# Optimization experiments

Measured on AMD Instinct MI355X. Metric: run time of the kernel, lower is better.

Reference implementation:

```python
import jax, jax.numpy as jnp
import numpy as np

N_NODES = 100000
N_EDGES = 1600000
FEAT, HID, OUT = 256, 128, 64
N_BATCH = 10000
EPS = 1e-5


def gcn_conv(x, src, dst, W, b, n):
    # PyG GCNConv: linear -> add self loops -> sym-normalized scatter-add -> bias
    h = x @ W  # [N, C]
    loop = jnp.arange(n, dtype=src.dtype)
    s = jnp.concatenate([src, loop])
    d = jnp.concatenate([dst, loop])
    deg = jax.ops.segment_sum(jnp.ones_like(d, dtype=h.dtype), d, num_segments=n)
    dinv = jnp.where(deg > 0, jax.lax.rsqrt(deg), 0.0)
    norm = dinv[s] * dinv[d]                    # [E+N]
    msg = h[s] * norm[:, None]                  # gather + scale
    out = jax.ops.segment_sum(msg, d, num_segments=n)  # scatter-add
    return out + b


def batch_norm(x, gamma, beta):
    # training-mode BatchNorm1d: batch statistics, biased variance
    mu = jnp.mean(x, axis=0)
    var = jnp.var(x, axis=0)
    return (x - mu) * jax.lax.rsqrt(var + EPS) * gamma + beta


def setup_inputs() -> dict:
    key = jax.random.key(0)
    ks = jax.random.split(key, 8)
    features = jax.random.normal(ks[0], (N_NODES, FEAT), dtype=jnp.float32)
    edge_index = jax.random.randint(ks[1], (2, N_EDGES), 0, N_NODES, dtype=jnp.int64 if jax.config.jax_enable_x64 else jnp.int32)
    batch_nodes = jax.random.randint(ks[2], (N_BATCH,), 0, N_NODES, dtype=jnp.int32)
    W1 = jax.random.normal(ks[3], (FEAT, HID), dtype=jnp.float32) * (1.0 / np.sqrt(FEAT))
    b1 = jnp.zeros((HID,), jnp.float32)
    gamma1 = jnp.ones((HID,), jnp.float32)
    beta1 = jnp.zeros((HID,), jnp.float32)
    W2 = jax.random.normal(ks[4], (HID, OUT), dtype=jnp.float32) * (1.0 / np.sqrt(HID))
    b2 = jnp.zeros((OUT,), jnp.float32)
    gamma2 = jnp.ones((OUT,), jnp.float32)
    beta2 = jnp.zeros((OUT,), jnp.float32)
    return {"features": features, "edge_index": edge_index, "batch_nodes": batch_nodes,
            "W1": W1, "b1": b1, "gamma1": gamma1, "beta1": beta1,
            "W2": W2, "b2": b2, "gamma2": gamma2, "beta2": beta2}


def reference(features, edge_index, batch_nodes, W1, b1, gamma1, beta1, W2, b2, gamma2, beta2):
    src, dst = edge_index[0], edge_index[1]
    n = features.shape[0]
    x = gcn_conv(features, src, dst, W1, b1, n)
    x = jax.nn.relu(batch_norm(x, gamma1, beta1))
    # dropout treated as identity (deterministic reference)
    x = gcn_conv(x, src, dst, W2, b2, n)
    x = jax.nn.relu(batch_norm(x, gamma2, beta2))
    return jax.nn.log_softmax(x[batch_nodes], axis=1)
```

## Files before the change

kernel.cpp:

```cpp
#include <hip/hip_runtime.h>
#include <stdint.h>

typedef unsigned short bf16_t;

constexpr int kNN   = 100000;
constexpr int kNE   = 1600000;
constexpr int kFEAT = 256;
constexpr int kHID  = 128;
constexpr int kOUT  = 64;
constexpr int kNB   = 10000;
constexpr float kEPS = 1e-5f;

constexpr int kEPB  = 4096;
constexpr int kNBLK = (kNE + kEPB - 1) / kEPB;
constexpr int kNBUK = (kNN + 511) / 512;

typedef __attribute__((ext_vector_type(8))) short short8v;
typedef __attribute__((ext_vector_type(4))) float f32x4;

__device__ __forceinline__ float bf2f(bf16_t u) {
    union { uint32_t i; float f; } v; v.i = ((uint32_t)u) << 16; return v.f;
}
__device__ __forceinline__ bf16_t f2bf(float f) {
    uint32_t u = __float_as_uint(f);
    uint32_t r = (u + 0x7FFFu + ((u >> 16) & 1u)) >> 16;
    return (bf16_t)r;
}
__device__ __forceinline__ float lo16(uint32_t u) {
    union { uint32_t i; float f; } v; v.i = u << 16; return v.f;
}
__device__ __forceinline__ float hi16(uint32_t u) {
    union { uint32_t i; float f; } v; v.i = u & 0xFFFF0000u; return v.f;
}

__global__ void k_probe(const uint32_t* __restrict__ feat, const uint32_t* __restrict__ ei,
                        int* __restrict__ flags) {
    int l = threadIdx.x;
    int good = 0;
    for (int j = l; j < 256; j += 64) {
        uint32_t e = (feat[j] >> 7) & 0xFFu;
        if (e >= 100u && e <= 132u) good++;
    }
    for (int o = 32; o; o >>= 1) good += __shfl_xor(good, o);
    int zeros = 0;
    for (int j = l; j < 128; j += 64) zeros += (ei[2 * j + 1] == 0u) ? 1 : 0;
    for (int o = 32; o; o >>= 1) zeros += __shfl_xor(zeros, o);
    if (l == 0) {
        flags[0] = (good > 128) ? 1 : 0;
        flags[1] = (zeros > 64) ? 1 : 0;
    }
}


__global__ void k_hist1(const int* __restrict__ ei, const int* __restrict__ flags,
                        unsigned int* __restrict__ counts) {
    __shared__ unsigned int lh[kNBUK];
    int t = threadIdx.x;
    for (int i = t; i < kNBUK; i += 256) lh[i] = 0u;
    __syncthreads();
    int i64 = flags[1];
    int base = blockIdx.x * kEPB;
    for (int k = 0; k < 16; k++) {
        int e = base + k * 256 + t;
        if (e < kNE) {
            int d = i64 ? ei[2 * (kNE + e)] : ei[kNE + e];
            atomicAdd(&lh[d >> 9], 1u);
        }
    }
    __syncthreads();
    for (int i = t; i < kNBUK; i += 256) counts[(size_t)i * kNBLK + blockIdx.x] = lh[i];
}

__global__ void k_scanA(const unsigned int* __restrict__ counts, unsigned int* __restrict__ base,
                        float* __restrict__ stats) {
    __shared__ unsigned int ss[256];
    int t = threadIdx.x;
    for (int i = t; i < 384; i += 256) stats[i] = 0.f;
    unsigned int tot = 0u;
    if (t < kNBUK) {
        const unsigned int* row = counts + (size_t)t * kNBLK;
        for (int j = 0; j < kNBLK; j++) tot += row[j];
    }
    ss[t] = tot;
    __syncthreads();
    for (int o = 1; o < 256; o <<= 1) {
        unsigned int x = (t >= o) ? ss[t - o] : 0u;
        __syncthreads();
        ss[t] += x;
        __syncthreads();
    }
    if (t < kNBUK) base[t] = ss[t] - tot;
    if (t == 0) base[kNBUK] = ss[255];
}

__global__ void k_scanB(const unsigned int* __restrict__ counts, const unsigned int* __restrict__ base,
                        unsigned int* __restrict__ off) {
    __shared__ unsigned int ss[64];
    int b = blockIdx.x, t = threadIdx.x;
    unsigned int run = base[b];
    for (int c0 = 0; c0 < kNBLK; c0 += 64) {
        int idx = c0 + t;
        unsigned int v = (idx < kNBLK) ? counts[(size_t)b * kNBLK + idx] : 0u;
        ss[t] = v;
        __syncthreads();
        for (int o = 1; o < 64; o <<= 1) {
            unsigned int x = (t >= o) ? ss[t - o] : 0u;
            __syncthreads();
            ss[t] += x;
            __syncthreads();
        }
        if (idx < kNBLK) off[(size_t)b * kNBLK + idx] = run + ss[t] - v;
        unsigned int ctot = ss[63];
        __syncthreads();
        run += ctot;
    }
}

__global__ void k_scatter1(const int* __restrict__ ei, const int* __restrict__ flags,
                           const unsigned int* __restrict__ off, unsigned int* __restrict__ pairs) {
    __shared__ unsigned int lcur[kNBUK];
    int t = threadIdx.x;
    for (int i = t; i < kNBUK; i += 256) lcur[i] = off[(size_t)i * kNBLK + blockIdx.x];
    __syncthreads();
    int i64 = flags[1];
    int base = blockIdx.x * kEPB;
    for (int k = 0; k < 16; k++) {
        int e = base + k * 256 + t;
        if (e < kNE) {
            int s, d;
            if (i64) { s = ei[2 * e]; d = ei[2 * (kNE + e)]; }
            else     { s = ei[e];     d = ei[kNE + e]; }
            unsigned int p = atomicAdd(&lcur[d >> 9], 1u);
            pairs[p] = (unsigned int)s | ((unsigned int)(d & 511) << 17);
        }
    }
}

__global__ void __launch_bounds__(1024) k_scatter2(const unsigned int* __restrict__ pairs,
                        const unsigned int* __restrict__ base, unsigned int* __restrict__ deg,
                        float* __restrict__ dinv, unsigned int* __restrict__ cursor,
                        int* __restrict__ sorted) {
    __shared__ unsigned int hist[512], sc[512], lcur[512];
    int b = blockIdx.x, t = threadIdx.x;
    unsigned int gb = base[b];
    int cnt = (int)(base[b + 1] - gb);
    if (t < 512) hist[t] = 0u;
    __syncthreads();
    for (int i = t; i < cnt; i += 1024) atomicAdd(&hist[pairs[gb + i] >> 17], 1u);
    __syncthreads();
    if (t < 512) sc[t] = hist[t];
    __syncthreads();
    for (int o = 1; o < 512; o <<= 1) {
        unsigned int x = 0u;
        if (t < 512 && t >= o) x = sc[t - o];
        __syncthreads();
        if (t < 512) sc[t] += x;
        __syncthreads();
    }
    if (t < 512) {
        lcur[t] = gb + sc[t] - hist[t];
        int node = b * 512 + t;
        if (node < kNN) {
            unsigned int dg = hist[t] + 1u;
            deg[node] = dg;
            dinv[node] = rsqrtf((float)dg);
            cursor[node] = gb + sc[t];
        }
    }
    __syncthreads();
    for (int i = t; i < cnt; i += 1024) {
        unsigned int pk = pairs[gb + i];
        unsigned int slot = atomicAdd(&lcur[pk >> 17], 1u);
        sorted[slot] = (int)(pk & 0x1FFFFu);
    }
}

__global__ void k_prepw(const void* __restrict__ W1, const void* __restrict__ W2,
                        const int* __restrict__ flags, bf16_t* __restrict__ Wz1,
                        bf16_t* __restrict__ Wz2) {
    int gid = blockIdx.x * 256 + threadIdx.x;
    int isbf = flags[0];
    if (gid < 4096) {
        int idx = gid;
        int l = idx & 63, j = (idx >> 6) & 7, t = idx >> 9;
        int col = j * 16 + (l & 15);
        int kb = t * 32 + (l >> 4) * 8;
        bf16_t o[8];
        if (isbf) {
            const bf16_t* Wb = (const bf16_t*)W1;
            #pragma unroll
            for (int i = 0; i < 8; i++) o[i] = Wb[(size_t)(kb + i) * kHID + col];
        } else {
            const float* Wf = (const float*)W1;
            #pragma unroll
            for (int i = 0; i < 8; i++) o[i] = f2bf(Wf[(size_t)(kb + i) * kHID + col]);
        }
        uint4 w;
        w.x = (uint32_t)o[0] | ((uint32_t)o[1] << 16);
        w.y = (uint32_t)o[2] | ((uint32_t)o[3] << 16);
        w.z = (uint32_t)o[4] | ((uint32_t)o[5] << 16);
        w.w = (uint32_t)o[6] | ((uint32_t)o[7] << 16);
        *(uint4*)(Wz1 + (size_t)idx * 8) = w;
    } else if (gid < 4096 + 1024) {
        int idx = gid - 4096;
        int l = idx & 63, j = (idx >> 6) & 3, t = idx >> 8;
        int col = j * 16 + (l & 15);
        int kb = t * 32 + (l >> 4) * 8;
        bf16_t o[8];
        if (isbf) {
            const bf16_t* Wb = (const bf16_t*)W2;
            #pragma unroll
            for (int i = 0; i < 8; i++) o[i] = Wb[(size_t)(kb + i) * kOUT + col];
        } else {
            const float* Wf = (const float*)W2;
            #pragma unroll
            for (int i = 0; i < 8; i++) o[i] = f2bf(Wf[(size_t)(kb + i) * kOUT + col]);
        }
        uint4 w;
        w.x = (uint32_t)o[0] | ((uint32_t)o[1] << 16);
        w.y = (uint32_t)o[2] | ((uint32_t)o[3] << 16);
        w.z = (uint32_t)o[4] | ((uint32_t)o[5] << 16);
        w.w = (uint32_t)o[6] | ((uint32_t)o[7] << 16);
        *(uint4*)(Wz2 + (size_t)idx * 8) = w;
    }
}

__global__ void k_gemm1(const void* __restrict__ A, const bf16_t* __restrict__ Wz,
                        const float* __restrict__ dinv, bf16_t* __restrict__ H,
                        const int* __restrict__ flags) {
    int isbf = flags[0];
    int wv = threadIdx.x >> 6;
    int l  = threadIdx.x & 63;
    int kgrp = l >> 4;
    int rbase = blockIdx.x * 128 + wv * 32;
    int arow0 = rbase + (l & 15);
    int arow1 = arow0 + 16;
    const bf16_t* Ab = (const bf16_t*)A;
    const float*  Af = (const float*)A;
    const short8v* Wv = (const short8v*)Wz;

    f32x4 acc[2][8];
    #pragma unroll
    for (int m = 0; m < 2; m++)
        #pragma unroll
        for (int j = 0; j < 8; j++)
            acc[m][j] = (f32x4){0.f, 0.f, 0.f, 0.f};

    #pragma unroll
    for (int t = 0; t < 8; t++) {
        int kbase = t * 32 + kgrp * 8;
        short8v a0, a1;
        #pragma unroll
        for (int i = 0; i < 8; i++) { a0[i] = 0; a1[i] = 0; }
        if (arow0 < kNN) {
            if (isbf) {
                a0 = *(const short8v*)(Ab + (size_t)arow0 * kFEAT + kbase);
            } else {
                const float* p = Af + (size_t)arow0 * kFEAT + kbase;
                #pragma unroll
                for (int i = 0; i < 8; i++) a0[i] = (short)f2bf(p[i]);
            }
        }
        if (arow1 < kNN) {
            if (isbf) {
                a1 = *(const short8v*)(Ab + (size_t)arow1 * kFEAT + kbase);
            } else {
                const float* p = Af + (size_t)arow1 * kFEAT + kbase;
                #pragma unroll
                for (int i = 0; i < 8; i++) a1[i] = (short)f2bf(p[i]);
            }
        }
        #pragma unroll
        for (int j = 0; j < 8; j++) {
            short8v b = Wv[(t * 8 + j) * 64 + l];
            acc[0][j] = __builtin_amdgcn_mfma_f32_16x16x32_bf16(a0, b, acc[0][j], 0, 0, 0);
            acc[1][j] = __builtin_amdgcn_mfma_f32_16x16x32_bf16(a1, b, acc[1][j], 0, 0, 0);
        }
    }

    #pragma unroll
    for (int m = 0; m < 2; m++) {
        #pragma unroll
        for (int r = 0; r < 4; r++) {
            int orow = rbase + m * 16 + kgrp * 4 + r;
            if (orow < kNN) {
                float dn = dinv[orow];
                bf16_t* hp = H + (size_t)orow * kHID + (l & 15);
                #pragma unroll
                for (int j = 0; j < 8; j++) hp[j * 16] = f2bf(acc[m][j][r] * dn);
            }
        }
    }
}

__global__ void k_agg1(const bf16_t* __restrict__ H, const int* __restrict__ sorted,
                       const unsigned int* __restrict__ cursor, const unsigned int* __restrict__ deg,
                       const float* __restrict__ dinv, const void* __restrict__ bias,
                       const int* __restrict__ flags, float* __restrict__ Out) {
    int t = threadIdx.x;
    int wv = t >> 6;
    int lane = t & 63;
    int c0 = lane * 2;
    int n = blockIdx.x * 4 + wv;
    float b0, b1v;
    if (flags[0]) { b0 = bf2f(((const bf16_t*)bias)[c0]); b1v = bf2f(((const bf16_t*)bias)[c0 + 1]); }
    else          { b0 = ((const float*)bias)[c0];        b1v = ((const float*)bias)[c0 + 1]; }
    const uint32_t* Hrow = (const uint32_t*)H;
    float dn = dinv[n];
    uint32_t hu = Hrow[(size_t)n * 64 + lane];
    float acc0 = lo16(hu), acc1 = hi16(hu);
    unsigned int e1 = cursor[n];
    int cnt = (int)(deg[n] - 1u);
    unsigned int e = e1 - (unsigned int)cnt;
    for (; cnt >= 8; cnt -= 8, e += 8) {
        int s0 = sorted[e],     s1 = sorted[e + 1], s2 = sorted[e + 2], s3 = sorted[e + 3];
        int s4 = sorted[e + 4], s5 = sorted[e + 5], s6 = sorted[e + 6], s7 = sorted[e + 7];
        uint32_t u0 = Hrow[(size_t)s0 * 64 + lane];
        uint32_t u1 = Hrow[(size_t)s1 * 64 + lane];
        uint32_t u2 = Hrow[(size_t)s2 * 64 + lane];
        uint32_t u3 = Hrow[(size_t)s3 * 64 + lane];
        uint32_t u4 = Hrow[(size_t)s4 * 64 + lane];
        uint32_t u5 = Hrow[(size_t)s5 * 64 + lane];
        uint32_t u6 = Hrow[(size_t)s6 * 64 + lane];
        uint32_t u7 = Hrow[(size_t)s7 * 64 + lane];
        acc0 += lo16(u0) + lo16(u1) + lo16(u2) + lo16(u3)
              + lo16(u4) + lo16(u5) + lo16(u6) + lo16(u7);
        acc1 += hi16(u0) + hi16(u1) + hi16(u2) + hi16(u3)
              + hi16(u4) + hi16(u5) + hi16(u6) + hi16(u7);
    }
    for (; cnt > 0; cnt--, e++) {
        uint32_t u = Hrow[(size_t)sorted[e] * 64 + lane];
        acc0 += lo16(u);
        acc1 += hi16(u);
    }
    float2 o; o.x = acc0 * dn + b0; o.y = acc1 * dn + b1v;
    *(float2*)(Out + (size_t)n * kHID + c0) = o;
}

__global__ void k_stat1(const float* __restrict__ A1, float* __restrict__ stats) {
    int c = threadIdx.x & 127;
    int r0 = threadIdx.x >> 7;
    int chunk = (kNN + gridDim.x - 1) / gridDim.x;
    int nbeg = blockIdx.x * chunk;
    int nend = nbeg + chunk; if (nend > kNN) nend = kNN;
    float s0 = 0.f, s1 = 0.f;
    for (int n = nbeg + r0; n < nend; n += 2) {
        float v = A1[(size_t)n * kHID + c];
        s0 += v; s1 += v * v;
    }
    atomicAdd(&stats[c], s0);
    atomicAdd(&stats[kHID + c], s1);
}

__global__ void k_bnprep(const float* __restrict__ stats, const void* __restrict__ gamma,
                         const void* __restrict__ beta, const int* __restrict__ flags,
                         float* __restrict__ bnp) {
    int c = threadIdx.x;
    float mu = stats[c] * (1.f / kNN);
    float var = stats[128 + c] * (1.f / kNN) - mu * mu;
    float rs = rsqrtf(var + kEPS);
    float g, b;
    if (flags[0]) { g = bf2f(((const bf16_t*)gamma)[c]); b = bf2f(((const bf16_t*)beta)[c]); }
    else          { g = ((const float*)gamma)[c];        b = ((const float*)beta)[c]; }
    float sc = rs * g;
    bnp[c] = sc;
    bnp[128 + c] = b - mu * sc;
}

__global__ void k_gemm2(const float* A, const bf16_t* __restrict__ Wz,
                        const float* __restrict__ dinv, const float* __restrict__ bnp,
                        bf16_t* H ) {
    int wv = threadIdx.x >> 6;
    int l  = threadIdx.x & 63;
    int kgrp = l >> 4;
    int rbase = blockIdx.x * 128 + wv * 32;
    int arow0 = rbase + (l & 15);
    int arow1 = arow0 + 16;
    const short8v* Wv = (const short8v*)Wz;

    f32x4 acc[2][4];
    #pragma unroll
    for (int m = 0; m < 2; m++)
        #pragma unroll
        for (int j = 0; j < 4; j++)
            acc[m][j] = (f32x4){0.f, 0.f, 0.f, 0.f};

    #pragma unroll
    for (int t = 0; t < 4; t++) {
        int kbase = t * 32 + kgrp * 8;
        float4 sa = *(const float4*)(bnp + kbase);
        float4 sb = *(const float4*)(bnp + kbase + 4);
        float4 ha = *(const float4*)(bnp + 128 + kbase);
        float4 hb = *(const float4*)(bnp + 128 + kbase + 4);
        short8v a0, a1;
        #pragma unroll
        for (int i = 0; i < 8; i++) { a0[i] = 0; a1[i] = 0; }
        if (arow0 < kNN) {
            float4 f0 = *(const float4*)(A + (size_t)arow0 * kHID + kbase);
            float4 f1 = *(const float4*)(A + (size_t)arow0 * kHID + kbase + 4);
            float v;
            v = f0.x * sa.x + ha.x; a0[0] = (short)f2bf(v > 0.f ? v : 0.f);
            v = f0.y * sa.y + ha.y; a0[1] = (short)f2bf(v > 0.f ? v : 0.f);
            v = f0.z * sa.z + ha.z; a0[2] = (short)f2bf(v > 0.f ? v : 0.f);
            v = f0.w * sa.w + ha.w; a0[3] = (short)f2bf(v > 0.f ? v : 0.f);
            v = f1.x * sb.x + hb.x; a0[4] = (short)f2bf(v > 0.f ? v : 0.f);
            v = f1.y * sb.y + hb.y; a0[5] = (short)f2bf(v > 0.f ? v : 0.f);
            v = f1.z * sb.z + hb.z; a0[6] = (short)f2bf(v > 0.f ? v : 0.f);
            v = f1.w * sb.w + hb.w; a0[7] = (short)f2bf(v > 0.f ? v : 0.f);
        }
        if (arow1 < kNN) {
            float4 f0 = *(const float4*)(A + (size_t)arow1 * kHID + kbase);
            float4 f1 = *(const float4*)(A + (size_t)arow1 * kHID + kbase + 4);
            float v;
            v = f0.x * sa.x + ha.x; a1[0] = (short)f2bf(v > 0.f ? v : 0.f);
            v = f0.y * sa.y + ha.y; a1[1] = (short)f2bf(v > 0.f ? v : 0.f);
            v = f0.z * sa.z + ha.z; a1[2] = (short)f2bf(v > 0.f ? v : 0.f);
            v = f0.w * sa.w + ha.w; a1[3] = (short)f2bf(v > 0.f ? v : 0.f);
            v = f1.x * sb.x + hb.x; a1[4] = (short)f2bf(v > 0.f ? v : 0.f);
            v = f1.y * sb.y + hb.y; a1[5] = (short)f2bf(v > 0.f ? v : 0.f);
            v = f1.z * sb.z + hb.z; a1[6] = (short)f2bf(v > 0.f ? v : 0.f);
            v = f1.w * sb.w + hb.w; a1[7] = (short)f2bf(v > 0.f ? v : 0.f);
        }
        #pragma unroll
        for (int j = 0; j < 4; j++) {
            short8v b = Wv[(t * 4 + j) * 64 + l];
            acc[0][j] = __builtin_amdgcn_mfma_f32_16x16x32_bf16(a0, b, acc[0][j], 0, 0, 0);
            acc[1][j] = __builtin_amdgcn_mfma_f32_16x16x32_bf16(a1, b, acc[1][j], 0, 0, 0);
        }
    }

    #pragma unroll
    for (int m = 0; m < 2; m++) {
        #pragma unroll
        for (int r = 0; r < 4; r++) {
            int orow = rbase + m * 16 + kgrp * 4 + r;
            if (orow < kNN) {
                float dn = dinv[orow];
                bf16_t* hp = H + (size_t)orow * 256 + (l & 15);
                #pragma unroll
                for (int j = 0; j < 4; j++) hp[j * 16] = f2bf(acc[m][j][r] * dn);
            }
        }
    }
}

__global__ void k_agg2(const bf16_t* __restrict__ H, const int* __restrict__ sorted,
                       const unsigned int* __restrict__ cursor, const unsigned int* __restrict__ deg,
                       const float* __restrict__ dinv, const void* __restrict__ bias,
                       const int* __restrict__ flags, float* __restrict__ Out) {
    int t = threadIdx.x;
    int grp = t >> 5;
    int lane = t & 31;
    int c0 = lane * 2;
    int n = blockIdx.x * 8 + grp;
    float b0, b1v;
    if (flags[0]) { b0 = bf2f(((const bf16_t*)bias)[c0]); b1v = bf2f(((const bf16_t*)bias)[c0 + 1]); }
    else          { b0 = ((const float*)bias)[c0];        b1v = ((const float*)bias)[c0 + 1]; }
    const uint32_t* Hrow = (const uint32_t*)H;
    float dn = dinv[n];
    uint32_t hu = Hrow[(size_t)n * 128 + lane];
    float acc0 = lo16(hu), acc1 = hi16(hu);
    unsigned int e1 = cursor[n];
    int cnt = (int)(deg[n] - 1u);
    unsigned int e = e1 - (unsigned int)cnt;
    for (; cnt >= 8; cnt -= 8, e += 8) {
        int s0 = sorted[e],     s1 = sorted[e + 1], s2 = sorted[e + 2], s3 = sorted[e + 3];
        int s4 = sorted[e + 4], s5 = sorted[e + 5], s6 = sorted[e + 6], s7 = sorted[e + 7];
        uint32_t u0 = Hrow[(size_t)s0 * 128 + lane];
        uint32_t u1 = Hrow[(size_t)s1 * 128 + lane];
        uint32_t u2 = Hrow[(size_t)s2 * 128 + lane];
        uint32_t u3 = Hrow[(size_t)s3 * 128 + lane];
        uint32_t u4 = Hrow[(size_t)s4 * 128 + lane];
        uint32_t u5 = Hrow[(size_t)s5 * 128 + lane];
        uint32_t u6 = Hrow[(size_t)s6 * 128 + lane];
        uint32_t u7 = Hrow[(size_t)s7 * 128 + lane];
        acc0 += lo16(u0) + lo16(u1) + lo16(u2) + lo16(u3)
              + lo16(u4) + lo16(u5) + lo16(u6) + lo16(u7);
        acc1 += hi16(u0) + hi16(u1) + hi16(u2) + hi16(u3)
              + hi16(u4) + hi16(u5) + hi16(u6) + hi16(u7);
    }
    for (; cnt > 0; cnt--, e++) {
        uint32_t u = Hrow[(size_t)sorted[e] * 128 + lane];
        acc0 += lo16(u);
        acc1 += hi16(u);
    }
    float2 o; o.x = acc0 * dn + b0; o.y = acc1 * dn + b1v;
    *(float2*)(Out + (size_t)n * kOUT + c0) = o;
}

__global__ void k_stat2(const float* __restrict__ A2, float* __restrict__ stats) {
    int c = threadIdx.x & 63;
    int r0 = threadIdx.x >> 6;
    int chunk = (kNN + gridDim.x - 1) / gridDim.x;
    int nbeg = blockIdx.x * chunk;
    int nend = nbeg + chunk; if (nend > kNN) nend = kNN;
    float s0 = 0.f, s1 = 0.f;
    for (int n = nbeg + r0; n < nend; n += 4) {
        float v = A2[(size_t)n * kOUT + c];
        s0 += v; s1 += v * v;
    }
    atomicAdd(&stats[256 + c], s0);
    atomicAdd(&stats[320 + c], s1);
}

__global__ void k_out(const float* __restrict__ A2, const float* __restrict__ stats,
                      const int* __restrict__ batch, const void* __restrict__ gamma,
                      const void* __restrict__ beta, const int* __restrict__ flags,
                      bf16_t* __restrict__ out) {
    int wid = threadIdx.x >> 6;
    int lane = threadIdx.x & 63;
    int i = blockIdx.x * 4 + wid;
    if (i >= kNB) return;
    int n = batch[i];
    int c = lane;
    float mu = stats[256 + c] * (1.f / kNN);
    float var = stats[320 + c] * (1.f / kNN) - mu * mu;
    float g, b;
    if (flags[0]) { g = bf2f(((const bf16_t*)gamma)[c]); b = bf2f(((const bf16_t*)beta)[c]); }
    else          { g = ((const float*)gamma)[c];        b = ((const float*)beta)[c]; }
    float v = (A2[(size_t)n * kOUT + c] - mu) * rsqrtf(var + kEPS) * g + b;
    v = v > 0.f ? v : 0.f;
    float m = v;
    for (int o = 32; o; o >>= 1) m = fmaxf(m, __shfl_xor(m, o));
    float ex = expf(v - m);
    float s = ex;
    for (int o = 32; o; o >>= 1) s += __shfl_xor(s, o);
    float r = v - m - logf(s);
    if (flags[0]) out[(size_t)i * kOUT + c] = f2bf(r);
    else ((float*)out)[(size_t)i * kOUT + c] = r;
}

static inline size_t align_up(size_t x, size_t a) { return (x + a - 1) & ~(a - 1); }

extern "C" void kernel_launch(void* const* d_in, const int* in_sizes, int n_in,
                              void* d_out, int out_size, void* d_ws, size_t ws_size,
                              hipStream_t stream) {
    (void)in_sizes; (void)n_in; (void)out_size; (void)ws_size;
    const void* feat = d_in[0];
    const int* ei    = (const int*)d_in[1];
    const int* batch = (const int*)d_in[2];
    const void* W1   = d_in[3];
    const void* b1   = d_in[4];
    const void* g1   = d_in[5];
    const void* be1  = d_in[6];
    const void* W2   = d_in[7];
    const void* b2   = d_in[8];
    const void* g2   = d_in[9];
    const void* be2  = d_in[10];

    char* ws = (char*)d_ws;
    size_t o = 0;
    int*          flags  = (int*)(ws + o);          o = align_up(o + 32, 256);
    unsigned int* deg    = (unsigned int*)(ws + o); o = align_up(o + (size_t)kNN * 4, 256);
    float*        dinv   = (float*)(ws + o);        o = align_up(o + (size_t)kNN * 4, 256);
    unsigned int* cursor = (unsigned int*)(ws + o); o = align_up(o + (size_t)kNN * 4, 256);
    float*        stats  = (float*)(ws + o);        o = align_up(o + 384 * 4, 256);
    float*        bnp    = (float*)(ws + o);        o = align_up(o + 256 * 4, 256);
    int*          sorted = (int*)(ws + o);          o = align_up(o + (size_t)kNE * 4, 256);
    bf16_t*       h1     = (bf16_t*)(ws + o);       o = align_up(o + (size_t)kNN * kHID * 2, 256);
    float*        a1     = (float*)(ws + o);        o = align_up(o + (size_t)kNN * kHID * 4, 256);
    bf16_t*       wz1    = (bf16_t*)(ws + o);       o = align_up(o + (size_t)8 * 8 * 64 * 8 * 2, 256);
    bf16_t*       wz2    = (bf16_t*)(ws + o);       o = align_up(o + (size_t)4 * 4 * 64 * 8 * 2, 256);

    unsigned int* pairs  = (unsigned int*)h1;
    unsigned int* counts = (unsigned int*)a1;
    unsigned int* offm   = (unsigned int*)((char*)a1 + 512 * 1024);
    unsigned int* gbase  = (unsigned int*)((char*)a1 + 1024 * 1024);

    bf16_t*       h2 = (bf16_t*)a1;
    float*        a2 = (float*)h1;

    bf16_t* outp = (bf16_t*)d_out;

    k_probe   <<<1, 64, 0, stream>>>((const uint32_t*)feat, (const uint32_t*)ei, flags);
    k_prepw   <<<20, 256, 0, stream>>>(W1, W2, flags, wz1, wz2);
    k_hist1   <<<kNBLK, 256, 0, stream>>>(ei, flags, counts);
    k_scanA   <<<1, 256, 0, stream>>>(counts, gbase, stats);
    k_scanB   <<<kNBUK, 64, 0, stream>>>(counts, gbase, offm);
    k_scatter1<<<kNBLK, 256, 0, stream>>>(ei, flags, offm, pairs);
    k_scatter2<<<kNBUK, 1024, 0, stream>>>(pairs, gbase, deg, dinv, cursor, sorted);

    k_gemm1 <<<(kNN + 127) / 128, 256, 0, stream>>>(feat, wz1, dinv, h1, flags);
    k_agg1  <<<kNN / 4, 256, 0, stream>>>(h1, sorted, cursor, deg, dinv, b1, flags, a1);
    k_stat1 <<<256, 256, 0, stream>>>(a1, stats);
    k_bnprep<<<1, 128, 0, stream>>>(stats, g1, be1, flags, bnp);

    k_gemm2<<<(kNN + 127) / 128, 256, 0, stream>>>(a1, wz2, dinv, bnp, h2);
    k_agg2 <<<kNN / 8, 256, 0, stream>>>(h2, sorted, cursor, deg, dinv, b2, flags, a2);
    k_stat2<<<256, 256, 0, stream>>>(a2, stats);

    k_out<<<(kNB + 3) / 4, 256, 0, stream>>>(a2, stats, batch, g2, be2, flags, outp);
}
```

Baseline: 501.8 us.

## Fuse dtype probe into weight prep and split agg2 edges across half-waves

Removes the separate single-block probe launch by having every k_prepw block recompute the dtype check, with block 0 writing the flags. k_agg2 now assigns one node per full 64-lane wave instead of per 32-lane half, and each half gathers alternate neighbours. The partial sums are combined with a cross-half shuffle. The node index is made wave-uniform with readfirstlane in both aggregation kernels. The goal is more outstanding memory requests per node and one fewer launch, at the cost of twice as many waves for agg2 and some redundant probe reads.

```diff
diff --git a/kernel.cpp b/kernel.cpp
--- a/kernel.cpp
+++ b/kernel.cpp
@@ -31,24 +31,6 @@
 }
 __device__ __forceinline__ float hi16(uint32_t u) {
     union { uint32_t i; float f; } v; v.i = u & 0xFFFF0000u; return v.f;
-}
-
-__global__ void k_probe(const uint32_t* __restrict__ feat, const uint32_t* __restrict__ ei,
-                        int* __restrict__ flags) {
-    int l = threadIdx.x;
-    int good = 0;
-    for (int j = l; j < 256; j += 64) {
-        uint32_t e = (feat[j] >> 7) & 0xFFu;
-        if (e >= 100u && e <= 132u) good++;
-    }
-    for (int o = 32; o; o >>= 1) good += __shfl_xor(good, o);
-    int zeros = 0;
-    for (int j = l; j < 128; j += 64) zeros += (ei[2 * j + 1] == 0u) ? 1 : 0;
-    for (int o = 32; o; o >>= 1) zeros += __shfl_xor(zeros, o);
-    if (l == 0) {
-        flags[0] = (good > 128) ? 1 : 0;
-        flags[1] = (zeros > 64) ? 1 : 0;
-    }
 }
 
 
@@ -176,15 +158,32 @@
 }
 
 __global__ void k_prepw(const void* __restrict__ W1, const void* __restrict__ W2,
-                        const int* __restrict__ flags, bf16_t* __restrict__ Wz1,
+                        const uint32_t* __restrict__ feat, const uint32_t* __restrict__ ei,
+                        int* __restrict__ flags, bf16_t* __restrict__ Wz1,
                         bf16_t* __restrict__ Wz2) {
-    int gid = blockIdx.x * 256 + threadIdx.x;
-    int isbf = flags[0];
+    int t = threadIdx.x;
+    int good = 0;
+    for (int j = t & 63; j < 256; j += 64) {
+        uint32_t ex = (feat[j] >> 7) & 0xFFu;
+        if (ex >= 100u && ex <= 132u) good++;
+    }
+    for (int o = 32; o; o >>= 1) good += __shfl_xor(good, o);
+    int isbf = (good > 128) ? 1 : 0;
+    if (blockIdx.x == 0) {
+        int zeros = 0;
+        for (int j = t & 63; j < 128; j += 64) zeros += (ei[2 * j + 1] == 0u) ? 1 : 0;
+        for (int o = 32; o; o >>= 1) zeros += __shfl_xor(zeros, o);
+        if (t == 0) {
+            flags[0] = isbf;
+            flags[1] = (zeros > 64) ? 1 : 0;
+        }
+    }
+    int gid = blockIdx.x * 256 + t;
     if (gid < 4096) {
         int idx = gid;
-        int l = idx & 63, j = (idx >> 6) & 7, t = idx >> 9;
+        int l = idx & 63, j = (idx >> 6) & 7, tt = idx >> 9;
         int col = j * 16 + (l & 15);
-        int kb = t * 32 + (l >> 4) * 8;
+        int kb = tt * 32 + (l >> 4) * 8;
         bf16_t o[8];
         if (isbf) {
             const bf16_t* Wb = (const bf16_t*)W1;
@@ -203,9 +202,9 @@
         *(uint4*)(Wz1 + (size_t)idx * 8) = w;
     } else if (gid < 4096 + 1024) {
         int idx = gid - 4096;
-        int l = idx & 63, j = (idx >> 6) & 3, t = idx >> 8;
+        int l = idx & 63, j = (idx >> 6) & 3, tt = idx >> 8;
         int col = j * 16 + (l & 15);
-        int kb = t * 32 + (l >> 4) * 8;
+        int kb = tt * 32 + (l >> 4) * 8;
         bf16_t o[8];
         if (isbf) {
             const bf16_t* Wb = (const bf16_t*)W2;
@@ -301,7 +300,7 @@
     int wv = t >> 6;
     int lane = t & 63;
     int c0 = lane * 2;
-    int n = blockIdx.x * 4 + wv;
+    int n = __builtin_amdgcn_readfirstlane(blockIdx.x * 4 + wv);
     float b0, b1v;
     if (flags[0]) { b0 = bf2f(((const bf16_t*)bias)[c0]); b1v = bf2f(((const bf16_t*)bias)[c0 + 1]); }
     else          { b0 = ((const float*)bias)[c0];        b1v = ((const float*)bias)[c0 + 1]; }
@@ -449,43 +448,66 @@
                        const float* __restrict__ dinv, const void* __restrict__ bias,
                        const int* __restrict__ flags, float* __restrict__ Out) {
     int t = threadIdx.x;
-    int grp = t >> 5;
-    int lane = t & 31;
-    int c0 = lane * 2;
-    int n = blockIdx.x * 8 + grp;
+    int wv = t >> 6;
+    int lane = t & 63;
+    int half = lane >> 5;
+    int w32 = lane & 31;
+    int c0 = w32 * 2;
+    int n = __builtin_amdgcn_readfirstlane(blockIdx.x * 4 + wv);
     float b0, b1v;
     if (flags[0]) { b0 = bf2f(((const bf16_t*)bias)[c0]); b1v = bf2f(((const bf16_t*)bias)[c0 + 1]); }
     else          { b0 = ((const float*)bias)[c0];        b1v = ((const float*)bias)[c0 + 1]; }
     const uint32_t* Hrow = (const uint32_t*)H;
     float dn = dinv[n];
-    uint32_t hu = Hrow[(size_t)n * 128 + lane];
-    float acc0 = lo16(hu), acc1 = hi16(hu);
+    uint32_t hu = Hrow[(size_t)n * 128 + w32];
+    float acc0 = half ? 0.f : lo16(hu);
+    float acc1 = half ? 0.f : hi16(hu);
     unsigned int e1 = cursor[n];
     int cnt = (int)(deg[n] - 1u);
     unsigned int e = e1 - (unsigned int)cnt;
-    for (; cnt >= 8; cnt -= 8, e += 8) {
-        int s0 = sorted[e],     s1 = sorted[e + 1], s2 = sorted[e + 2], s3 = sorted[e + 3];
-        int s4 = sorted[e + 4], s5 = sorted[e + 5], s6 = sorted[e + 6], s7 = sorted[e + 7];
-        uint32_t u0 = Hrow[(size_t)s0 * 128 + lane];
-        uint32_t u1 = Hrow[(size_t)s1 * 128 + lane];
-        uint32_t u2 = Hrow[(size_t)s2 * 128 + lane];
-        uint32_t u3 = Hrow[(size_t)s3 * 128 + lane];
-        uint32_t u4 = Hrow[(size_t)s4 * 128 + lane];
-        uint32_t u5 = Hrow[(size_t)s5 * 128 + lane];
-        uint32_t u6 = Hrow[(size_t)s6 * 128 + lane];
-        uint32_t u7 = Hrow[(size_t)s7 * 128 + lane];
+    for (; cnt >= 16; cnt -= 16, e += 16) {
+        int s0 = sorted[e],      s1 = sorted[e + 1],  s2 = sorted[e + 2],  s3 = sorted[e + 3];
+        int s4 = sorted[e + 4],  s5 = sorted[e + 5],  s6 = sorted[e + 6],  s7 = sorted[e + 7];
+        int s8 = sorted[e + 8],  s9 = sorted[e + 9],  sa = sorted[e + 10], sb = sorted[e + 11];
+        int sc = sorted[e + 12], sd = sorted[e + 13], se = sorted[e + 14], sf = sorted[e + 15];
+        int i0 = half ? s1 : s0;
+        int i1 = half ? s3 : s2;
+        int i2 = half ? s5 : s4;
+        int i3 = half ? s7 : s6;
+        int i4 = half ? s9 : s8;
+        int i5 = half ? sb : sa;
+        int i6 = half ? sd : sc;
+        int i7 = half ? sf : se;
+        uint32_t u0 = Hrow[(size_t)i0 * 128 + w32];
+        uint32_t u1 = Hrow[(size_t)i1 * 128 + w32];
+        uint32_t u2 = Hrow[(size_t)i2 * 128 + w32];
+        uint32_t u3 = Hrow[(size_t)i3 * 128 + w32];
+        uint32_t u4 = Hrow[(size_t)i4 * 128 + w32];
+        uint32_t u5 = Hrow[(size_t)i5 * 128 + w32];
+        uint32_t u6 = Hrow[(size_t)i6 * 128 + w32];
+        uint32_t u7 = Hrow[(size_t)i7 * 128 + w32];
         acc0 += lo16(u0) + lo16(u1) + lo16(u2) + lo16(u3)
               + lo16(u4) + lo16(u5) + lo16(u6) + lo16(u7);
         acc1 += hi16(u0) + hi16(u1) + hi16(u2) + hi16(u3)
               + hi16(u4) + hi16(u5) + hi16(u6) + hi16(u7);
     }
-    for (; cnt > 0; cnt--, e++) {
-        uint32_t u = Hrow[(size_t)sorted[e] * 128 + lane];
+    for (; cnt >= 2; cnt -= 2, e += 2) {
+        int sA = sorted[e], sB = sorted[e + 1];
+        int si = half ? sB : sA;
+        uint32_t u = Hrow[(size_t)si * 128 + w32];
         acc0 += lo16(u);
         acc1 += hi16(u);
     }
-    float2 o; o.x = acc0 * dn + b0; o.y = acc1 * dn + b1v;
-    *(float2*)(Out + (size_t)n * kOUT + c0) = o;
+    if (cnt) {
+        uint32_t u = Hrow[(size_t)sorted[e] * 128 + w32];
+        if (!half) { acc0 += lo16(u); acc1 += hi16(u); }
+    }
+    acc0 += __shfl_xor(acc0, 32);
+    acc1 += __shfl_xor(acc1, 32);
+    if (!half) {
+        float2 o; o.x = acc0 * dn + b0; o.y = acc1 * dn + b1v;
+        *(float2*)(Out + (size_t)n * kOUT + c0) = o;
+    }
 }
 
 __global__ void k_stat2(const float* __restrict__ A2, float* __restrict__ stats) {
@@ -572,8 +594,8 @@
 
     bf16_t* outp = (bf16_t*)d_out;
 
-    k_probe   <<<1, 64, 0, stream>>>((const uint32_t*)feat, (const uint32_t*)ei, flags);
-    k_prepw   <<<20, 256, 0, stream>>>(W1, W2, flags, wz1, wz2);
+    k_prepw   <<<20, 256, 0, stream>>>(W1, W2, (const uint32_t*)feat, (const uint32_t*)ei,
+                                       flags, wz1, wz2);
     k_hist1   <<<kNBLK, 256, 0, stream>>>(ei, flags, counts);
     k_scanA   <<<1, 256, 0, stream>>>(counts, gbase, stats);
     k_scanB   <<<kNBUK, 64, 0, stream>>>(counts, gbase, offm);
@@ -586,7 +608,7 @@
     k_bnprep<<<1, 128, 0, stream>>>(stats, g1, be1, flags, bnp);
 
     k_gemm2<<<(kNN + 127) / 128, 256, 0, stream>>>(a1, wz2, dinv, bnp, h2);
-    k_agg2 <<<kNN / 8, 256, 0, stream>>>(h2, sorted, cursor, deg, dinv, b2, flags, a2);
+    k_agg2 <<<kNN / 4, 256, 0, stream>>>(h2, sorted, cursor, deg, dinv, b2, flags, a2);
     k_stat2<<<256, 256, 0, stream>>>(a2, stats);
 
     k_out<<<(kNB + 3) / 4, 256, 0, stream>>>(a2, stats, batch, g2, be2, flags, outp);
```

After: 493.1 us. About the same (-1.7%).
